# Performance work log

Hardware: AMD Instinct MI355X
Metric: run time of the kernel (lower is better)

The kernel has to match this reference:

```python
import jax, jax.numpy as jnp
import numpy as np

T, B_SZ = 1024, 1024
NX, NU, ND, NM, NDT, NH = 128, 64, 32, 32, 32, 128


def setup_inputs() -> dict:
    key = jax.random.key(0)
    ks = jax.random.split(key, 10)
    return {
        "x": jax.random.normal(ks[0], (B_SZ, NX), jnp.float32),
        "M_flow": jax.random.normal(ks[1], (T, B_SZ, NM), jnp.float32),
        "DT": jax.random.normal(ks[2], (T, B_SZ, NDT), jnp.float32),
        "D": jax.random.normal(ks[3], (T, B_SZ, ND), jnp.float32),
        # ConstrainedLinear(nx, nx): weight and scalar init with torch.rand -> uniform[0,1)
        "A_weight": jax.random.uniform(ks[4], (NX, NX), jnp.float32),
        "A_scalar": jax.random.uniform(ks[5], (NX, NX), jnp.float32),
        # nn.Linear(in, out, bias=False) weights are [out, in]
        "B_w": jax.random.normal(ks[6], (NX, NU), jnp.float32) * (1.0 / np.sqrt(NU)),
        "E_w": jax.random.normal(ks[7], (NX, ND), jnp.float32) * (1.0 / np.sqrt(ND)),
        "hf1_w": jax.random.normal(ks[8], (NH, NM + NDT), jnp.float32) * (1.0 / np.sqrt(NM + NDT)),
        "hf2_w": jax.random.normal(ks[9], (NU, NH), jnp.float32) * (1.0 / np.sqrt(NH)),
    }


def reference(x, M_flow, DT, D, A_weight, A_scalar, B_w, E_w, hf1_w, hf2_w):
    # Constrained weight: ((1 - 0.1*sigmoid(scalar)) * softmax(weight, dim=1)).T
    # It is constant across time, so compute once (torch redundantly recomputes it per step).
    s_clamped = 1.0 - 0.1 * jax.nn.sigmoid(A_scalar)
    W_eff = (s_clamped * jax.nn.softmax(A_weight, axis=1)).T  # [nx, nx]

    # Per-step control input u_t depends only on exogenous M_flow/DT -> vectorize over time.
    md = jnp.concatenate([M_flow, DT], axis=2)                # [T, B, n_m+n_dT]
    h = jax.nn.relu(jnp.einsum('tbi,hi->tbh', md, hf1_w))     # [T, B, n_hidden]
    u = jax.nn.relu(jnp.einsum('tbh,uh->tbu', h, hf2_w))      # [T, B, nu]

    # Precompute additive drive B(u_t) + E(d_t); only x@W_eff is sequential.
    drive = jnp.einsum('tbu,xu->tbx', u, B_w) + jnp.einsum('tbd,xd->tbx', D, E_w)

    def step(x_prev, drive_t):
        x_new = x_prev @ W_eff + drive_t
        return x_new, x_new

    _, X = jax.lax.scan(step, x, drive)  # X: [T, B, nx]
    Y = X[:, :, -1]                      # [T, B]
    return X, Y
```

## Files before the change

### kernel.cpp

```cpp
#include <hip/hip_runtime.h>

typedef _Float16 h4 __attribute__((ext_vector_type(4)));
typedef _Float16 h8 __attribute__((ext_vector_type(8)));
typedef float f4 __attribute__((ext_vector_type(4)));

#define MFMA16(a, b, c) __builtin_amdgcn_mfma_f32_16x16x32_f16((a), (b), (c), 0, 0, 0)

static constexpr int TT  = 1024;
static constexpr int BS  = 1024;
static constexpr int LCH = 64;
static constexpr int NCH = 16;
static constexpr size_t XTOT = (size_t)TT * BS * 128;

static constexpr size_t WS_WT16 = 0;
static constexpr size_t WS_HF1  = 32768;
static constexpr size_t WS_HF2  = 49152;
static constexpr size_t WS_BW   = 65536;
static constexpr size_t WS_EW   = 81920;
static constexpr size_t WS_W64  = 122880;
static constexpr size_t WS_F    = 253952;
static constexpr size_t WS_INIT = WS_F + (size_t)NCH * BS * 128 * 4;
static constexpr size_t WS_DRV  = WS_INIT + (size_t)NCH * BS * 128 * 4;

template <typename T>
__device__ inline T ntload(const T* p) { return __builtin_nontemporal_load(p); }

__global__ void prep_kernel(const float* __restrict__ Aw, const float* __restrict__ As,
                            const float* __restrict__ hf1, const float* __restrict__ hf2,
                            const float* __restrict__ Bw, const float* __restrict__ Ew,
                            char* __restrict__ ws)
{
    const int tid = threadIdx.x;
    const int bid = blockIdx.x;
    if (bid < 128) {
        __shared__ float red[128];
        const int n = bid;
        const float a = Aw[n * 128 + tid];
        red[tid] = a;
        __syncthreads();
        for (int s = 64; s > 0; s >>= 1) {
            if (tid < s) red[tid] = fmaxf(red[tid], red[tid + s]);
            __syncthreads();
        }
        const float mx = red[0];
        __syncthreads();
        const float e = expf(a - mx);
        red[tid] = e;
        __syncthreads();
        for (int s = 64; s > 0; s >>= 1) {
            if (tid < s) red[tid] += red[tid + s];
            __syncthreads();
        }
        const float sm  = e / red[0];
        const float asv = As[n * 128 + tid];
        const float sc  = 1.0f - 0.1f * (1.0f / (1.0f + expf(-asv)));
        ((_Float16*)(ws + WS_WT16))[n * 128 + tid] = (_Float16)(sc * sm);
    } else {
        const int b2 = bid - 128;
        for (int i = b2 * 128 + tid; i < 8192; i += 32 * 128) {
            ((_Float16*)(ws + WS_HF1))[i] = (_Float16)hf1[i];
            ((_Float16*)(ws + WS_HF2))[i] = (_Float16)hf2[i];
            ((_Float16*)(ws + WS_BW))[i]  = (_Float16)Bw[i];
            if (i < 4096) ((_Float16*)(ws + WS_EW))[i] = (_Float16)Ew[i];
        }
    }
}

__global__ void w64_kernel(char* __restrict__ ws)
{
    const int tid  = threadIdx.x;
    const int lane = tid & 63;
    const int w    = tid >> 6;
    const int cl   = lane & 15;
    const int gq   = lane >> 4;

    __shared__ __align__(16) _Float16 Ta[128 * 128];
    __shared__ __align__(16) _Float16 Tb[128 * 128];

    const _Float16* Wt16 = (const _Float16*)(ws + WS_WT16);
    for (int i = tid; i < 2048; i += 256)
        *(h8*)&Ta[i * 8] = *(const h8*)&Wt16[i * 8];
    __syncthreads();

    for (int s = 0; s < 6; ++s) {
        const _Float16* src = (s & 1) ? Tb : Ta;
        _Float16* dst       = (s & 1) ? Ta : Tb;
        f4 acc[8][2];
#pragma unroll
        for (int mt = 0; mt < 8; ++mt)
#pragma unroll
            for (int nt = 0; nt < 2; ++nt) acc[mt][nt] = f4{};
#pragma unroll
        for (int kk = 0; kk < 4; ++kk) {
            h8 b0, b1;
#pragma unroll
            for (int j = 0; j < 8; ++j) {
                const int kr = kk * 32 + gq * 8 + j;
                b0[j] = src[kr * 128 + w * 32 + cl];
                b1[j] = src[kr * 128 + w * 32 + 16 + cl];
            }
#pragma unroll
            for (int mt = 0; mt < 8; ++mt) {
                h8 a = *(const h8*)&src[(mt * 16 + cl) * 128 + kk * 32 + gq * 8];
                acc[mt][0] = MFMA16(a, b0, acc[mt][0]);
                acc[mt][1] = MFMA16(a, b1, acc[mt][1]);
            }
        }
        __syncthreads();
#pragma unroll
        for (int mt = 0; mt < 8; ++mt)
#pragma unroll
            for (int nt = 0; nt < 2; ++nt)
#pragma unroll
                for (int r = 0; r < 4; ++r)
                    dst[(mt * 16 + gq * 4 + r) * 128 + w * 32 + nt * 16 + cl] =
                        (_Float16)acc[mt][nt][r];
        __syncthreads();
    }
    _Float16* W64 = (_Float16*)(ws + WS_W64);
    for (int i = tid; i < 2048; i += 256)
        *(h8*)&W64[i * 8] = *(const h8*)&Ta[i * 8];
}

__global__ __launch_bounds__(256, 4)
void drive_kernel(const float* __restrict__ Mfl, const float* __restrict__ DTi,
                  const float* __restrict__ Din, char* __restrict__ ws, int t0)
{
    const int tid  = threadIdx.x;
    const int lane = tid & 63;
    const int w    = tid >> 6;
    const int cl   = lane & 15;
    const int gq   = lane >> 4;
    const int bt   = blockIdx.x & 63;
    const int tq   = blockIdx.x >> 6;
    const int b0   = bt * 16;

    const _Float16* Hf1  = (const _Float16*)(ws + WS_HF1);
    const _Float16* Hf2  = (const _Float16*)(ws + WS_HF2);
    const _Float16* Bw16 = (const _Float16*)(ws + WS_BW);
    const _Float16* Ew16 = (const _Float16*)(ws + WS_EW);
    _Float16* Drv        = (_Float16*)(ws + WS_DRV);

    __shared__ __align__(16) _Float16 mds[4][16 * 64];
    __shared__ __align__(16) _Float16 dts[4][16 * 32];
    __shared__ __align__(16) _Float16 hs[4][16 * 128];
    __shared__ __align__(16) _Float16 us[4][16 * 64];

    const int qrow = (tid & 127) >> 3;
    const int qc4  = (tid & 7) * 4;
    f4 pm[4], pd[4];
#pragma unroll
    for (int s = 0; s < 4; ++s) {
        const size_t t  = (size_t)(t0 + tq * 4 + s);
        const size_t rb = (t * BS + b0 + qrow) * 32 + qc4;
        pm[s] = (tid < 128) ? ntload((const f4*)&Mfl[rb]) : ntload((const f4*)&DTi[rb]);
        if (tid < 128) pd[s] = ntload((const f4*)&Din[rb]);
    }
#pragma unroll
    for (int s = 0; s < 4; ++s) {
        const int col = (tid < 128) ? qc4 : (32 + qc4);
        h4 hv;
#pragma unroll
        for (int j = 0; j < 4; ++j) hv[j] = (_Float16)pm[s][j];
        *(h4*)&mds[s][qrow * 64 + (((col >> 3) ^ (qrow & 7)) * 8) + (col & 7)] = hv;
        if (tid < 128) {
            h4 h2;
#pragma unroll
            for (int j = 0; j < 4; ++j) h2[j] = (_Float16)pd[s][j];
            *(h4*)&dts[s][qrow * 32 + (((qc4 >> 3) ^ (qrow & 3)) * 8) + (qc4 & 7)] = h2;
        }
    }

    h8 hf1f[2][2], bwf[2][2], ewf[2], hf2f[4];
#pragma unroll
    for (int nt = 0; nt < 2; ++nt) {
        const int ng = w * 32 + nt * 16 + cl;
#pragma unroll
        for (int kk = 0; kk < 2; ++kk) {
            hf1f[nt][kk] = *(const h8*)&Hf1[ng * 64 + kk * 32 + gq * 8];
            bwf[nt][kk]  = *(const h8*)&Bw16[ng * 64 + kk * 32 + gq * 8];
        }
        ewf[nt] = *(const h8*)&Ew16[ng * 32 + gq * 8];
    }
    {
        const int ng = w * 16 + cl;
#pragma unroll
        for (int kk = 0; kk < 4; ++kk)
            hf2f[kk] = *(const h8*)&Hf2[ng * 128 + kk * 32 + gq * 8];
    }
    __syncthreads();

#pragma unroll
    for (int s = 0; s < 4; ++s) {
        f4 ha[2] = {};
#pragma unroll
        for (int kk = 0; kk < 2; ++kk) {
            h8 a = *(const h8*)&mds[s][cl * 64 + (((kk * 4 + gq) ^ (cl & 7)) * 8)];
            ha[0] = MFMA16(a, hf1f[0][kk], ha[0]);
            ha[1] = MFMA16(a, hf1f[1][kk], ha[1]);
        }
#pragma unroll
        for (int nt = 0; nt < 2; ++nt) {
            const int colg = w * 32 + nt * 16 + cl;
#pragma unroll
            for (int r = 0; r < 4; ++r) {
                const int row = gq * 4 + r;
                hs[s][row * 128 + (((colg >> 3) ^ (row & 15)) * 8) + (colg & 7)] =
                    (_Float16)fmaxf(ha[nt][r], 0.f);
            }
        }
    }
    __syncthreads();

#pragma unroll
    for (int s = 0; s < 4; ++s) {
        f4 ua = {};
#pragma unroll
        for (int kk = 0; kk < 4; ++kk) {
            h8 a = *(const h8*)&hs[s][cl * 128 + (((kk * 4 + gq) ^ (cl & 15)) * 8)];
            ua = MFMA16(a, hf2f[kk], ua);
        }
        const int colg = w * 16 + cl;
#pragma unroll
        for (int r = 0; r < 4; ++r) {
            const int row = gq * 4 + r;
            us[s][row * 64 + (((colg >> 3) ^ (row & 7)) * 8) + (colg & 7)] =
                (_Float16)fmaxf(ua[r], 0.f);
        }
    }
    __syncthreads();

#pragma unroll
    for (int s = 0; s < 4; ++s) {
        f4 acc[2] = {};
#pragma unroll
        for (int kk = 0; kk < 2; ++kk) {
            h8 a = *(const h8*)&us[s][cl * 64 + (((kk * 4 + gq) ^ (cl & 7)) * 8)];
            acc[0] = MFMA16(a, bwf[0][kk], acc[0]);
            acc[1] = MFMA16(a, bwf[1][kk], acc[1]);
        }
        {
            h8 a = *(const h8*)&dts[s][cl * 32 + ((gq ^ (cl & 3)) * 8)];
            acc[0] = MFMA16(a, ewf[0], acc[0]);
            acc[1] = MFMA16(a, ewf[1], acc[1]);
        }
        h8 hv;
#pragma unroll
        for (int nt = 0; nt < 2; ++nt)
#pragma unroll
            for (int r = 0; r < 4; ++r) hv[nt * 4 + r] = (_Float16)acc[nt][r];
        const size_t tl = (size_t)tq * 4 + s;
        *(h8*)&Drv[((tl * 64 + bt) * 256 + tid) * 8] = hv;
    }
}

template <bool FINAL>
__global__ __launch_bounds__(256, 4)
void scan_kernel(char* __restrict__ ws, int c0, float* __restrict__ Xout,
                 float* __restrict__ Yout)
{
    const int tid  = threadIdx.x;
    const int lane = tid & 63;
    const int w    = tid >> 6;
    const int cl   = lane & 15;
    const int gq   = lane >> 4;
    const int bt   = blockIdx.x & 63;
    const int cg   = c0 + (blockIdx.x >> 6);
    const int cloc = cg & 7;
    const int b0   = bt * 16;

    const _Float16* Wt16 = (const _Float16*)(ws + WS_WT16);
    const _Float16* Drv  = (const _Float16*)(ws + WS_DRV);
    float* Fbuf          = (float*)(ws + WS_F);
    const float* Init    = (const float*)(ws + WS_INIT);

    __shared__ __align__(16) _Float16 xs[2][16 * 128];

    h8 wtf[2][4];
#pragma unroll
    for (int nt = 0; nt < 2; ++nt) {
        const int ng = w * 32 + nt * 16 + cl;
#pragma unroll
        for (int kk = 0; kk < 4; ++kk)
            wtf[nt][kk] = *(const h8*)&Wt16[ng * 128 + kk * 32 + gq * 8];
    }

    if constexpr (FINAL) {
        const int row = tid >> 4, c8 = tid & 15;
        const float* src = &Init[((size_t)cg * BS + b0 + row) * 128 + c8 * 8];
        f4 v0 = *(const f4*)src;
        f4 v1 = *(const f4*)(src + 4);
        h8 hv;
#pragma unroll
        for (int j = 0; j < 4; ++j) { hv[j] = (_Float16)v0[j]; hv[4 + j] = (_Float16)v1[j]; }
        *(h8*)&xs[0][row * 128 + ((c8 ^ row) & 15) * 8] = hv;
    } else {
        h8 z = {};
        *(h8*)&xs[0][tid * 8] = z;
    }
    __syncthreads();

    const size_t doff = (size_t)cloc * 64 * 131072 + (size_t)bt * 2048 + (size_t)tid * 8;
    auto LD = [&](int k) -> h8 { return *(const h8*)&Drv[doff + (size_t)k * 131072]; };

    int cur = 0;
    auto step = [&](int k, const h8& dc) {
        f4 acc[2];
#pragma unroll
        for (int nt = 0; nt < 2; ++nt)
#pragma unroll
            for (int r = 0; r < 4; ++r) acc[nt][r] = (float)dc[nt * 4 + r];

#pragma unroll
        for (int kk = 0; kk < 4; ++kk) {
            h8 a = *(const h8*)&xs[cur][cl * 128 + (((kk * 4 + gq) ^ (cl & 15)) * 8)];
            acc[0] = MFMA16(a, wtf[0][kk], acc[0]);
            acc[1] = MFMA16(a, wtf[1][kk], acc[1]);
        }

        const int nxt = cur ^ 1;
        if constexpr (FINAL) {
            const size_t t = (size_t)cg * LCH + k;
#pragma unroll
            for (int nt = 0; nt < 2; ++nt) {
                const int colg = w * 32 + nt * 16 + cl;
#pragma unroll
                for (int r = 0; r < 4; ++r) {
                    const int row = gq * 4 + r;
                    const float v = acc[nt][r];
                    __builtin_nontemporal_store(v, &Xout[(t * BS + b0 + row) * 128 + colg]);
                    xs[nxt][row * 128 + (((colg >> 3) ^ (row & 15)) * 8) + (colg & 7)] =
                        (_Float16)v;
                }
            }
            if (w == 3 && cl == 15) {
#pragma unroll
                for (int r = 0; r < 4; ++r)
                    __builtin_nontemporal_store(acc[1][r], &Yout[t * BS + b0 + gq * 4 + r]);
            }
        } else {
            if (k == LCH - 1) {
#pragma unroll
                for (int nt = 0; nt < 2; ++nt) {
                    const int colg = w * 32 + nt * 16 + cl;
#pragma unroll
                    for (int r = 0; r < 4; ++r) {
                        const int row = gq * 4 + r;
                        Fbuf[((size_t)cg * BS + b0 + row) * 128 + colg] = acc[nt][r];
                    }
                }
            } else {
#pragma unroll
                for (int nt = 0; nt < 2; ++nt) {
                    const int colg = w * 32 + nt * 16 + cl;
#pragma unroll
                    for (int r = 0; r < 4; ++r) {
                        const int row = gq * 4 + r;
                        xs[nxt][row * 128 + (((colg >> 3) ^ (row & 15)) * 8) + (colg & 7)] =
                            (_Float16)acc[nt][r];
                    }
                }
            }
        }
        __syncthreads();
        cur = nxt;
    };

    h8 dc0 = LD(0);
    h8 dc1 = LD(1);
    for (int k = 0; k < LCH; k += 2) {
        {
            h8 d = dc0;
            if (k + 2 < LCH) dc0 = LD(k + 2);
            step(k, d);
        }
        {
            h8 d = dc1;
            if (k + 3 < LCH) dc1 = LD(k + 3);
            step(k + 1, d);
        }
    }
}

__global__ __launch_bounds__(256, 2)
void carry_kernel(const float* __restrict__ x0, char* __restrict__ ws,
                  int cc_lo, int cc_hi, int copy0)
{
    const int tid  = threadIdx.x;
    const int lane = tid & 63;
    const int w    = tid >> 6;
    const int cl   = lane & 15;
    const int gq   = lane >> 4;
    const int b0   = blockIdx.x * 16;

    const _Float16* W64 = (const _Float16*)(ws + WS_W64);
    const float* Fbuf   = (const float*)(ws + WS_F);
    float* Init         = (float*)(ws + WS_INIT);

    __shared__ __align__(16) _Float16 xs[2][16 * 128];

    h8 wlf[2][4];
#pragma unroll
    for (int nt = 0; nt < 2; ++nt) {
        const int ng = w * 32 + nt * 16 + cl;
#pragma unroll
        for (int kk = 0; kk < 4; ++kk)
            wlf[nt][kk] = *(const h8*)&W64[ng * 128 + kk * 32 + gq * 8];
    }

    {
        const int row = tid >> 4, c8 = tid & 15;
        const float* src = &x0[(b0 + row) * 128 + c8 * 8];
        f4 v0 = *(const f4*)src, v1 = *(const f4*)(src + 4);
        if (copy0) {
            float* dst = &Init[((size_t)cc_lo * BS + b0 + row) * 128 + c8 * 8];
            *(f4*)dst = v0;
            *(f4*)(dst + 4) = v1;
        }
        h8 hv;
#pragma unroll
        for (int j = 0; j < 4; ++j) { hv[j] = (_Float16)v0[j]; hv[4 + j] = (_Float16)v1[j]; }
        *(h8*)&xs[0][row * 128 + ((c8 ^ row) & 15) * 8] = hv;
    }
    __syncthreads();

    int cur = 0;
    for (int cc = cc_lo + 1; cc <= cc_hi; ++cc) {
        f4 acc[2] = {};
#pragma unroll
        for (int kk = 0; kk < 4; ++kk) {
            h8 a = *(const h8*)&xs[cur][cl * 128 + (((kk * 4 + gq) ^ (cl & 15)) * 8)];
            acc[0] = MFMA16(a, wlf[0][kk], acc[0]);
            acc[1] = MFMA16(a, wlf[1][kk], acc[1]);
        }
        const int nxt = cur ^ 1;
#pragma unroll
        for (int nt = 0; nt < 2; ++nt) {
            const int colg = w * 32 + nt * 16 + cl;
#pragma unroll
            for (int r = 0; r < 4; ++r) {
                const int row = gq * 4 + r;
                const float v =
                    acc[nt][r] + Fbuf[((size_t)(cc - 1) * BS + b0 + row) * 128 + colg];
                Init[((size_t)cc * BS + b0 + row) * 128 + colg] = v;
                xs[nxt][row * 128 + (((colg >> 3) ^ (row & 15)) * 8) + (colg & 7)] =
                    (_Float16)v;
            }
        }
        __syncthreads();
        cur = nxt;
    }
}

extern "C" void kernel_launch(void* const* d_in, const int* in_sizes, int n_in,
                              void* d_out, int out_size, void* d_ws, size_t ws_size,
                              hipStream_t stream)
{
    const float* x_in = (const float*)d_in[0];
    const float* Mfl  = (const float*)d_in[1];
    const float* DTi  = (const float*)d_in[2];
    const float* Din  = (const float*)d_in[3];
    const float* Aw   = (const float*)d_in[4];
    const float* As   = (const float*)d_in[5];
    const float* Bw   = (const float*)d_in[6];
    const float* Ew   = (const float*)d_in[7];
    const float* hf1  = (const float*)d_in[8];
    const float* hf2  = (const float*)d_in[9];
    char* ws    = (char*)d_ws;
    float* Xout = (float*)d_out;
    float* Yout = Xout + XTOT;
    const float* Init8 = (const float*)(ws + WS_INIT) + (size_t)8 * BS * 128;

    prep_kernel<<<dim3(160), dim3(128), 0, stream>>>(Aw, As, hf1, hf2, Bw, Ew, ws);
    w64_kernel<<<dim3(1), dim3(256), 0, stream>>>(ws);

    drive_kernel<<<dim3(128 * 64), dim3(256), 0, stream>>>(Mfl, DTi, Din, ws, 0);
    scan_kernel<false><<<dim3(8 * 64), dim3(256), 0, stream>>>(ws, 0, nullptr, nullptr);
    carry_kernel<<<dim3(64), dim3(256), 0, stream>>>(x_in, ws, 0, 8, 1);
    scan_kernel<true><<<dim3(8 * 64), dim3(256), 0, stream>>>(ws, 0, Xout, Yout);

    drive_kernel<<<dim3(128 * 64), dim3(256), 0, stream>>>(Mfl, DTi, Din, ws, 512);
    scan_kernel<false><<<dim3(7 * 64), dim3(256), 0, stream>>>(ws, 8, nullptr, nullptr);
    carry_kernel<<<dim3(64), dim3(256), 0, stream>>>(Init8, ws, 8, 15, 0);
    scan_kernel<true><<<dim3(8 * 64), dim3(256), 0, stream>>>(ws, 8, Xout, Yout);
}
```

Before: 435.0 us.

## Halve scan chunk length and run each batch tile in a single wave

Cuts the chunk length from 64 to 32 steps, doubling the number of chunks so more independent chunk scans run in parallel. The carry step now uses W^32, computed with one fewer squaring. The scan and carry kernels switch to one wave per 16-row batch tile holding all of W in registers, so block-wide barriers are no longer needed per step. The drive kernel stores its output in a layout that matches the new per-wave reads. In exchange the carry kernel has twice as many serial steps, and each wave needs many more registers.

New measurement: 502.6 us. +15.5%, slower.

```diff
diff --git a/kernel.cpp b/kernel.cpp
--- a/kernel.cpp
+++ b/kernel.cpp
@@ -8,8 +8,8 @@
 
 static constexpr int TT  = 1024;
 static constexpr int BS  = 1024;
-static constexpr int LCH = 64;
-static constexpr int NCH = 16;
+static constexpr int LCH = 32;
+static constexpr int NCH = 32;
 static constexpr size_t XTOT = (size_t)TT * BS * 128;
 
 static constexpr size_t WS_WT16 = 0;
@@ -17,8 +17,8 @@
 static constexpr size_t WS_HF2  = 49152;
 static constexpr size_t WS_BW   = 65536;
 static constexpr size_t WS_EW   = 81920;
-static constexpr size_t WS_W64  = 122880;
-static constexpr size_t WS_F    = 253952;
+static constexpr size_t WS_W32  = 90112;
+static constexpr size_t WS_F    = 131072;
 static constexpr size_t WS_INIT = WS_F + (size_t)NCH * BS * 128 * 4;
 static constexpr size_t WS_DRV  = WS_INIT + (size_t)NCH * BS * 128 * 4;
 
@@ -66,7 +66,7 @@
     }
 }
 
-__global__ void w64_kernel(char* __restrict__ ws)
+__global__ void w32_kernel(char* __restrict__ ws)
 {
     const int tid  = threadIdx.x;
     const int lane = tid & 63;
@@ -82,7 +82,7 @@
         *(h8*)&Ta[i * 8] = *(const h8*)&Wt16[i * 8];
     __syncthreads();
 
-    for (int s = 0; s < 6; ++s) {
+    for (int s = 0; s < 5; ++s) {
         const _Float16* src = (s & 1) ? Tb : Ta;
         _Float16* dst       = (s & 1) ? Ta : Tb;
         f4 acc[8][2];
@@ -117,9 +117,9 @@
                         (_Float16)acc[mt][nt][r];
         __syncthreads();
     }
-    _Float16* W64 = (_Float16*)(ws + WS_W64);
+    _Float16* W32 = (_Float16*)(ws + WS_W32);
     for (int i = tid; i < 2048; i += 256)
-        *(h8*)&W64[i * 8] = *(const h8*)&Ta[i * 8];
+        *(h8*)&W32[i * 8] = *(const h8*)&Tb[i * 8];
 }
 
 __global__ __launch_bounds__(256, 4)
@@ -244,211 +244,208 @@
             acc[0] = MFMA16(a, ewf[0], acc[0]);
             acc[1] = MFMA16(a, ewf[1], acc[1]);
         }
-        h8 hv;
-#pragma unroll
-        for (int nt = 0; nt < 2; ++nt)
-#pragma unroll
-            for (int r = 0; r < 4; ++r) hv[nt * 4 + r] = (_Float16)acc[nt][r];
-        const size_t tl = (size_t)tq * 4 + s;
-        *(h8*)&Drv[((tl * 64 + bt) * 256 + tid) * 8] = hv;
+#pragma unroll
+        for (int nt = 0; nt < 2; ++nt) {
+            const int n = w * 32 + nt * 16 + cl;
+#pragma unroll
+            for (int r = 0; r < 4; ++r) {
+                const int b = gq * 4 + r;
+                hs[s][b * 128 + (((n >> 3) ^ b) & 15) * 8 + (n & 7)] = (_Float16)acc[nt][r];
+            }
+        }
+    }
+    __syncthreads();
+
+    {
+        const int s2 = tid >> 6;
+        const int l2 = tid & 63, c2 = l2 & 15, g2 = l2 >> 4;
+        const size_t tl = (size_t)tq * 4 + s2;
+        _Float16* dst = &Drv[(((size_t)tl * 64 + bt) * 64 + l2) * 32];
+#pragma unroll
+        for (int p = 0; p < 4; ++p) {
+            h4 lo = *(const h4*)&hs[s2][c2 * 128 + (((4 * p + (g2 >> 1)) ^ c2) & 15) * 8 + (g2 & 1) * 4];
+            h4 hi = *(const h4*)&hs[s2][c2 * 128 + (((4 * p + 2 + (g2 >> 1)) ^ c2) & 15) * 8 + (g2 & 1) * 4];
+            h8 o;
+#pragma unroll
+            for (int j = 0; j < 4; ++j) { o[j] = lo[j]; o[4 + j] = hi[j]; }
+            *(h8*)&dst[p * 8] = o;
+        }
     }
 }
 
 template <bool FINAL>
-__global__ __launch_bounds__(256, 4)
-void scan_kernel(char* __restrict__ ws, int c0, float* __restrict__ Xout,
-                 float* __restrict__ Yout)
-{
-    const int tid  = threadIdx.x;
-    const int lane = tid & 63;
-    const int w    = tid >> 6;
-    const int cl   = lane & 15;
-    const int gq   = lane >> 4;
-    const int bt   = blockIdx.x & 63;
-    const int cg   = c0 + (blockIdx.x >> 6);
-    const int cloc = cg & 7;
-    const int b0   = bt * 16;
+__global__ __launch_bounds__(128, 1)
+void scan_kernel(char* __restrict__ ws, int c0,
+                 float* __restrict__ Xout, float* __restrict__ Yout)
+{
+    const int wslot = threadIdx.x >> 6;
+    const int wid   = blockIdx.x * 2 + wslot;
+    const int lane  = threadIdx.x & 63;
+    const int cl = lane & 15, gq = lane >> 4;
+    const int c  = c0 + (wid >> 6);
+    const int bt = wid & 63;
+    const int b0 = bt * 16;
+    const int cloc = c & 15;
 
     const _Float16* Wt16 = (const _Float16*)(ws + WS_WT16);
     const _Float16* Drv  = (const _Float16*)(ws + WS_DRV);
-    float* Fbuf          = (float*)(ws + WS_F);
-    const float* Init    = (const float*)(ws + WS_INIT);
-
-    __shared__ __align__(16) _Float16 xs[2][16 * 128];
-
-    h8 wtf[2][4];
-#pragma unroll
-    for (int nt = 0; nt < 2; ++nt) {
-        const int ng = w * 32 + nt * 16 + cl;
-#pragma unroll
-        for (int kk = 0; kk < 4; ++kk)
-            wtf[nt][kk] = *(const h8*)&Wt16[ng * 128 + kk * 32 + gq * 8];
-    }
-
+    float* Fbuf       = (float*)(ws + WS_F);
+    const float* Init = (const float*)(ws + WS_INIT);
+
+    __shared__ __align__(16) _Float16 tb[2][16 * 128];
+    _Float16* tbuf = tb[wslot];
+
+    h8 wf[8][4];
+#pragma unroll
+    for (int nt = 0; nt < 8; ++nt)
+#pragma unroll
+        for (int kt = 0; kt < 4; ++kt)
+            wf[nt][kt] = *(const h8*)&Wt16[(nt * 16 + cl) * 128 + kt * 32 + gq * 8];
+
+    h8 xf[4];
     if constexpr (FINAL) {
-        const int row = tid >> 4, c8 = tid & 15;
-        const float* src = &Init[((size_t)cg * BS + b0 + row) * 128 + c8 * 8];
-        f4 v0 = *(const f4*)src;
-        f4 v1 = *(const f4*)(src + 4);
-        h8 hv;
-#pragma unroll
-        for (int j = 0; j < 4; ++j) { hv[j] = (_Float16)v0[j]; hv[4 + j] = (_Float16)v1[j]; }
-        *(h8*)&xs[0][row * 128 + ((c8 ^ row) & 15) * 8] = hv;
+        f4 iv[8];
+#pragma unroll
+        for (int nt = 0; nt < 8; ++nt)
+            iv[nt] = *(const f4*)&Init[((size_t)c * BS + b0 + cl) * 128 + nt * 16 + gq * 4];
+#pragma unroll
+        for (int nt = 0; nt < 8; ++nt) {
+            h4 hv;
+#pragma unroll
+            for (int r = 0; r < 4; ++r) hv[r] = (_Float16)iv[nt][r];
+            *(h4*)&tbuf[cl * 128 + (((nt * 2 + (gq >> 1)) ^ cl) & 15) * 8 + (gq & 1) * 4] = hv;
+        }
+#pragma unroll
+        for (int kt = 0; kt < 4; ++kt)
+            xf[kt] = *(const h8*)&tbuf[cl * 128 + (((kt * 4 + gq) ^ cl) & 15) * 8];
     } else {
-        h8 z = {};
-        *(h8*)&xs[0][tid * 8] = z;
-    }
-    __syncthreads();
-
-    const size_t doff = (size_t)cloc * 64 * 131072 + (size_t)bt * 2048 + (size_t)tid * 8;
-    auto LD = [&](int k) -> h8 { return *(const h8*)&Drv[doff + (size_t)k * 131072]; };
-
-    int cur = 0;
-    auto step = [&](int k, const h8& dc) {
-        f4 acc[2];
-#pragma unroll
-        for (int nt = 0; nt < 2; ++nt)
-#pragma unroll
-            for (int r = 0; r < 4; ++r) acc[nt][r] = (float)dc[nt * 4 + r];
-
-#pragma unroll
-        for (int kk = 0; kk < 4; ++kk) {
-            h8 a = *(const h8*)&xs[cur][cl * 128 + (((kk * 4 + gq) ^ (cl & 15)) * 8)];
-            acc[0] = MFMA16(a, wtf[0][kk], acc[0]);
-            acc[1] = MFMA16(a, wtf[1][kk], acc[1]);
-        }
-
-        const int nxt = cur ^ 1;
+#pragma unroll
+        for (int kt = 0; kt < 4; ++kt) xf[kt] = h8{};
+    }
+
+    const h8* dp = (const h8*)&Drv[(((size_t)cloc * 32 * 64 + bt) * 64 + lane) * 32];
+    h8 dr[4];
+#pragma unroll
+    for (int p = 0; p < 4; ++p) dr[p] = dp[p];
+
+    for (int k = 0; k < LCH; ++k) {
+        f4 acc[8];
+#pragma unroll
+        for (int p = 0; p < 4; ++p)
+#pragma unroll
+            for (int r = 0; r < 4; ++r) {
+                acc[2 * p][r]     = (float)dr[p][r];
+                acc[2 * p + 1][r] = (float)dr[p][4 + r];
+            }
+        if (k + 1 < LCH) {
+            const h8* np = dp + (size_t)(k + 1) * 16384;
+#pragma unroll
+            for (int p = 0; p < 4; ++p) dr[p] = np[p];
+        }
+#pragma unroll
+        for (int kt = 0; kt < 4; ++kt)
+#pragma unroll
+            for (int nt = 0; nt < 8; ++nt)
+                acc[nt] = MFMA16(wf[nt][kt], xf[kt], acc[nt]);
+
         if constexpr (FINAL) {
-            const size_t t = (size_t)cg * LCH + k;
-#pragma unroll
-            for (int nt = 0; nt < 2; ++nt) {
-                const int colg = w * 32 + nt * 16 + cl;
-#pragma unroll
-                for (int r = 0; r < 4; ++r) {
-                    const int row = gq * 4 + r;
-                    const float v = acc[nt][r];
-                    __builtin_nontemporal_store(v, &Xout[(t * BS + b0 + row) * 128 + colg]);
-                    xs[nxt][row * 128 + (((colg >> 3) ^ (row & 15)) * 8) + (colg & 7)] =
-                        (_Float16)v;
-                }
-            }
-            if (w == 3 && cl == 15) {
-#pragma unroll
-                for (int r = 0; r < 4; ++r)
-                    __builtin_nontemporal_store(acc[1][r], &Yout[t * BS + b0 + gq * 4 + r]);
-            }
-        } else {
-            if (k == LCH - 1) {
-#pragma unroll
-                for (int nt = 0; nt < 2; ++nt) {
-                    const int colg = w * 32 + nt * 16 + cl;
-#pragma unroll
-                    for (int r = 0; r < 4; ++r) {
-                        const int row = gq * 4 + r;
-                        Fbuf[((size_t)cg * BS + b0 + row) * 128 + colg] = acc[nt][r];
-                    }
-                }
-            } else {
-#pragma unroll
-                for (int nt = 0; nt < 2; ++nt) {
-                    const int colg = w * 32 + nt * 16 + cl;
-#pragma unroll
-                    for (int r = 0; r < 4; ++r) {
-                        const int row = gq * 4 + r;
-                        xs[nxt][row * 128 + (((colg >> 3) ^ (row & 15)) * 8) + (colg & 7)] =
-                            (_Float16)acc[nt][r];
-                    }
-                }
-            }
-        }
-        __syncthreads();
-        cur = nxt;
-    };
-
-    h8 dc0 = LD(0);
-    h8 dc1 = LD(1);
-    for (int k = 0; k < LCH; k += 2) {
-        {
-            h8 d = dc0;
-            if (k + 2 < LCH) dc0 = LD(k + 2);
-            step(k, d);
-        }
-        {
-            h8 d = dc1;
-            if (k + 3 < LCH) dc1 = LD(k + 3);
-            step(k + 1, d);
-        }
-    }
-}
-
-__global__ __launch_bounds__(256, 2)
+            const size_t t = (size_t)c * LCH + k;
+            float* xp = &Xout[(t * BS + b0 + cl) * 128 + gq * 4];
+#pragma unroll
+            for (int nt = 0; nt < 8; ++nt)
+                __builtin_nontemporal_store(acc[nt], (f4*)&xp[nt * 16]);
+            if (gq == 3)
+                __builtin_nontemporal_store(acc[7][3], &Yout[t * BS + b0 + cl]);
+        } else if (k == LCH - 1) {
+#pragma unroll
+            for (int nt = 0; nt < 8; ++nt)
+                *(f4*)&Fbuf[((size_t)c * BS + b0 + cl) * 128 + nt * 16 + gq * 4] = acc[nt];
+        }
+        if (k < LCH - 1) {
+#pragma unroll
+            for (int nt = 0; nt < 8; ++nt) {
+                h4 hv;
+#pragma unroll
+                for (int r = 0; r < 4; ++r) hv[r] = (_Float16)acc[nt][r];
+                *(h4*)&tbuf[cl * 128 + (((nt * 2 + (gq >> 1)) ^ cl) & 15) * 8 + (gq & 1) * 4] = hv;
+            }
+#pragma unroll
+            for (int kt = 0; kt < 4; ++kt)
+                xf[kt] = *(const h8*)&tbuf[cl * 128 + (((kt * 4 + gq) ^ cl) & 15) * 8];
+        }
+    }
+}
+
+__global__ __launch_bounds__(64, 1)
 void carry_kernel(const float* __restrict__ x0, char* __restrict__ ws,
-                  int cc_lo, int cc_hi, int copy0)
-{
-    const int tid  = threadIdx.x;
-    const int lane = tid & 63;
-    const int w    = tid >> 6;
-    const int cl   = lane & 15;
-    const int gq   = lane >> 4;
-    const int b0   = blockIdx.x * 16;
-
-    const _Float16* W64 = (const _Float16*)(ws + WS_W64);
+                  int cc_lo, int n_steps, int copy0)
+{
+    const int lane = threadIdx.x;
+    const int cl = lane & 15, gq = lane >> 4;
+    const int b0 = blockIdx.x * 16;
+
+    const _Float16* W32 = (const _Float16*)(ws + WS_W32);
     const float* Fbuf   = (const float*)(ws + WS_F);
     float* Init         = (float*)(ws + WS_INIT);
 
-    __shared__ __align__(16) _Float16 xs[2][16 * 128];
-
-    h8 wlf[2][4];
-#pragma unroll
-    for (int nt = 0; nt < 2; ++nt) {
-        const int ng = w * 32 + nt * 16 + cl;
-#pragma unroll
-        for (int kk = 0; kk < 4; ++kk)
-            wlf[nt][kk] = *(const h8*)&W64[ng * 128 + kk * 32 + gq * 8];
-    }
-
+    __shared__ __align__(16) _Float16 tbuf[16 * 128];
+
+    h8 wf[8][4];
+#pragma unroll
+    for (int nt = 0; nt < 8; ++nt)
+#pragma unroll
+        for (int kt = 0; kt < 4; ++kt)
+            wf[nt][kt] = *(const h8*)&W32[(nt * 16 + cl) * 128 + kt * 32 + gq * 8];
+
+    h8 xf[4];
     {
-        const int row = tid >> 4, c8 = tid & 15;
-        const float* src = &x0[(b0 + row) * 128 + c8 * 8];
-        f4 v0 = *(const f4*)src, v1 = *(const f4*)(src + 4);
+        f4 iv[8];
+#pragma unroll
+        for (int nt = 0; nt < 8; ++nt)
+            iv[nt] = *(const f4*)&x0[(size_t)(b0 + cl) * 128 + nt * 16 + gq * 4];
         if (copy0) {
-            float* dst = &Init[((size_t)cc_lo * BS + b0 + row) * 128 + c8 * 8];
-            *(f4*)dst = v0;
-            *(f4*)(dst + 4) = v1;
-        }
-        h8 hv;
-#pragma unroll
-        for (int j = 0; j < 4; ++j) { hv[j] = (_Float16)v0[j]; hv[4 + j] = (_Float16)v1[j]; }
-        *(h8*)&xs[0][row * 128 + ((c8 ^ row) & 15) * 8] = hv;
-    }
-    __syncthreads();
-
-    int cur = 0;
-    for (int cc = cc_lo + 1; cc <= cc_hi; ++cc) {
-        f4 acc[2] = {};
-#pragma unroll
-        for (int kk = 0; kk < 4; ++kk) {
-            h8 a = *(const h8*)&xs[cur][cl * 128 + (((kk * 4 + gq) ^ (cl & 15)) * 8)];
-            acc[0] = MFMA16(a, wlf[0][kk], acc[0]);
-            acc[1] = MFMA16(a, wlf[1][kk], acc[1]);
-        }
-        const int nxt = cur ^ 1;
-#pragma unroll
-        for (int nt = 0; nt < 2; ++nt) {
-            const int colg = w * 32 + nt * 16 + cl;
-#pragma unroll
-            for (int r = 0; r < 4; ++r) {
-                const int row = gq * 4 + r;
-                const float v =
-                    acc[nt][r] + Fbuf[((size_t)(cc - 1) * BS + b0 + row) * 128 + colg];
-                Init[((size_t)cc * BS + b0 + row) * 128 + colg] = v;
-                xs[nxt][row * 128 + (((colg >> 3) ^ (row & 15)) * 8) + (colg & 7)] =
-                    (_Float16)v;
-            }
-        }
-        __syncthreads();
-        cur = nxt;
+#pragma unroll
+            for (int nt = 0; nt < 8; ++nt)
+                *(f4*)&Init[((size_t)cc_lo * BS + b0 + cl) * 128 + nt * 16 + gq * 4] = iv[nt];
+        }
+#pragma unroll
+        for (int nt = 0; nt < 8; ++nt) {
+            h4 hv;
+#pragma unroll
+            for (int r = 0; r < 4; ++r) hv[r] = (_Float16)iv[nt][r];
+            *(h4*)&tbuf[cl * 128 + (((nt * 2 + (gq >> 1)) ^ cl) & 15) * 8 + (gq & 1) * 4] = hv;
+        }
+#pragma unroll
+        for (int kt = 0; kt < 4; ++kt)
+            xf[kt] = *(const h8*)&tbuf[cl * 128 + (((kt * 4 + gq) ^ cl) & 15) * 8];
+    }
+
+    for (int i = 1; i <= n_steps; ++i) {
+        const int cc = cc_lo + i;
+        f4 acc[8];
+#pragma unroll
+        for (int nt = 0; nt < 8; ++nt)
+            acc[nt] = *(const f4*)&Fbuf[((size_t)(cc - 1) * BS + b0 + cl) * 128 + nt * 16 + gq * 4];
+#pragma unroll
+        for (int kt = 0; kt < 4; ++kt)
+#pragma unroll
+            for (int nt = 0; nt < 8; ++nt)
+                acc[nt] = MFMA16(wf[nt][kt], xf[kt], acc[nt]);
+#pragma unroll
+        for (int nt = 0; nt < 8; ++nt)
+            *(f4*)&Init[((size_t)cc * BS + b0 + cl) * 128 + nt * 16 + gq * 4] = acc[nt];
+        if (i < n_steps) {
+#pragma unroll
+            for (int nt = 0; nt < 8; ++nt) {
+                h4 hv;
+#pragma unroll
+                for (int r = 0; r < 4; ++r) hv[r] = (_Float16)acc[nt][r];
+                *(h4*)&tbuf[cl * 128 + (((nt * 2 + (gq >> 1)) ^ cl) & 15) * 8 + (gq & 1) * 4] = hv;
+            }
+#pragma unroll
+            for (int kt = 0; kt < 4; ++kt)
+                xf[kt] = *(const h8*)&tbuf[cl * 128 + (((kt * 4 + gq) ^ cl) & 15) * 8];
+        }
     }
 }
 
@@ -469,18 +466,18 @@
     char* ws    = (char*)d_ws;
     float* Xout = (float*)d_out;
     float* Yout = Xout + XTOT;
-    const float* Init8 = (const float*)(ws + WS_INIT) + (size_t)8 * BS * 128;
+    const float* Init16 = (const float*)(ws + WS_INIT) + (size_t)16 * BS * 128;
 
     prep_kernel<<<dim3(160), dim3(128), 0, stream>>>(Aw, As, hf1, hf2, Bw, Ew, ws);
-    w64_kernel<<<dim3(1), dim3(256), 0, stream>>>(ws);
+    w32_kernel<<<dim3(1), dim3(256), 0, stream>>>(ws);
 
     drive_kernel<<<dim3(128 * 64), dim3(256), 0, stream>>>(Mfl, DTi, Din, ws, 0);
-    scan_kernel<false><<<dim3(8 * 64), dim3(256), 0, stream>>>(ws, 0, nullptr, nullptr);
-    carry_kernel<<<dim3(64), dim3(256), 0, stream>>>(x_in, ws, 0, 8, 1);
-    scan_kernel<true><<<dim3(8 * 64), dim3(256), 0, stream>>>(ws, 0, Xout, Yout);
+    scan_kernel<false><<<dim3(512), dim3(128), 0, stream>>>(ws, 0, nullptr, nullptr);
+    carry_kernel<<<dim3(64), dim3(64), 0, stream>>>(x_in, ws, 0, 16, 1);
+    scan_kernel<true><<<dim3(512), dim3(128), 0, stream>>>(ws, 0, Xout, Yout);
 
     drive_kernel<<<dim3(128 * 64), dim3(256), 0, stream>>>(Mfl, DTi, Din, ws, 512);
-    scan_kernel<false><<<dim3(7 * 64), dim3(256), 0, stream>>>(ws, 8, nullptr, nullptr);
-    carry_kernel<<<dim3(64), dim3(256), 0, stream>>>(Init8, ws, 8, 15, 0);
-    scan_kernel<true><<<dim3(8 * 64), dim3(256), 0, stream>>>(ws, 8, Xout, Yout);
-}
+    scan_kernel<false><<<dim3(480), dim3(128), 0, stream>>>(ws, 16, nullptr, nullptr);
+    carry_kernel<<<dim3(64), dim3(64), 0, stream>>>(Init16, ws, 16, 15, 0);
+    scan_kernel<true><<<dim3(512), dim3(128), 0, stream>>>(ws, 16, Xout, Yout);
+}
```
